# Kernel tuning notes

Hardware: AMD Instinct MI355X
Metric: run time of the kernel (lower is better)

## Reference

```python
import jax, jax.numpy as jnp
import numpy as np

N_NODES = 50000
N_EDGES = 1200000
F_IN = 128
F_EDGE = 32
H = 78


def _p(key, shape, fan_in):
    return jax.random.normal(key, shape, dtype=jnp.float32) / np.sqrt(fan_in)


def setup_inputs() -> dict:
    key = jax.random.key(0)
    ks = jax.random.split(key, 20)
    x = jax.random.normal(ks[0], (N_NODES, F_IN), dtype=jnp.float32)
    edge_index = jax.random.randint(ks[1], (2, N_EDGES), 0, N_NODES, dtype=jnp.int32)
    edge_attr = jax.random.normal(ks[2], (N_EDGES, F_EDGE), dtype=jnp.float32)
    return {
        "x": x, "edge_index": edge_index, "edge_attr": edge_attr,
        # GATConv layer 1
        "W1": _p(ks[3], (F_IN, H), F_IN), "as1": _p(ks[4], (H,), H), "ad1": _p(ks[5], (H,), H),
        "b1": jnp.zeros((H,), jnp.float32),
        # GATConv layer 2
        "W2": _p(ks[6], (H, H), H), "as2": _p(ks[7], (H,), H), "ad2": _p(ks[8], (H,), H),
        "b2": jnp.zeros((H,), jnp.float32),
        # edge MLP
        "Wm1": _p(ks[9], (F_EDGE, H), F_EDGE), "bm1": jnp.zeros((H,), jnp.float32),
        "Wm2": _p(ks[10], (H, H), H), "bm2": jnp.zeros((H,), jnp.float32),
        # final edge head
        "Wf": _p(ks[11], (3 * H, 1), 3 * H), "bf": jnp.zeros((1,), jnp.float32),
    }


def _gat_conv(x, W, a_src, a_dst, bias, src, dst, n_nodes):
    """PyG GATConv, heads=1, negative_slope=0.2, self-loops already in src/dst."""
    h = x @ W                                   # [N, H]
    alpha_s = h @ a_src                         # [N]
    alpha_d = h @ a_dst                         # [N]
    e = jax.nn.leaky_relu(alpha_s[src] + alpha_d[dst], negative_slope=0.2)  # [E']
    # softmax over incoming edges per destination node
    m = jax.ops.segment_max(e, dst, num_segments=n_nodes)
    e = jnp.exp(e - m[dst])
    s = jax.ops.segment_sum(e, dst, num_segments=n_nodes)
    alpha = e / (s[dst] + 1e-16)                # [E']
    out = jax.ops.segment_sum(alpha[:, None] * h[src], dst, num_segments=n_nodes)
    return out + bias


def reference(x, edge_index, edge_attr, W1, as1, ad1, b1, W2, as2, ad2, b2,
              Wm1, bm1, Wm2, bm2, Wf, bf):
    n_nodes = x.shape[0]
    loop = jnp.arange(n_nodes, dtype=edge_index.dtype)
    src = jnp.concatenate([edge_index[0], loop])  # add self-loops (PyG default)
    dst = jnp.concatenate([edge_index[1], loop])

    h = _gat_conv(x, W1, as1, ad1, b1, src, dst, n_nodes)
    h = jax.nn.relu(h)  # dropout is identity in eval mode
    h = _gat_conv(h, W2, as2, ad2, b2, src, dst, n_nodes)

    ef = jax.nn.relu(edge_attr @ Wm1 + bm1) @ Wm2 + bm2            # [E, H]
    emb = jnp.concatenate([h[edge_index[0]], h[edge_index[1]], ef], axis=1)  # [E, 3H]
    return jnp.squeeze(emb @ Wf + bf, axis=-1)                     # [E]
```

## Files before the change

kernel.cpp:

```cpp
#include <hip/hip_runtime.h>
#include <math.h>

#define NN 50000
#define NE 1200000
#define FIN 128
#define FE 32
#define H 78
#define HP 80
#define ETOT (NE + NN)

#define NPB 64
#define NBUCK ((NN + NPB - 1) / NPB)
#define BCAP 2560

#define EB 6400
#define NBE ((ETOT + EB - 1) / EB)
#define GHN (NBUCK * NBE)
#define GS_NB ((GHN + 1023) / 1024)

typedef __attribute__((ext_vector_type(8))) short bf16x8;
typedef __attribute__((ext_vector_type(4))) float f32x4;

__device__ __forceinline__ unsigned short f2bf(float f) {
  unsigned u = __float_as_uint(f);
  return (unsigned short)((u + 0x7FFFu + ((u >> 16) & 1u)) >> 16);
}
__device__ __forceinline__ float bf2f(unsigned short b) {
  return __uint_as_float((unsigned)b << 16);
}

union Frag { uint4 q; bf16x8 v; unsigned short u[8]; };

__global__ void wperm_build(const float* __restrict__ W, int K, int steps,
                            uint4* __restrict__ out) {
  int idx = blockIdx.x * blockDim.x + threadIdx.x;
  int total = steps * 5 * 2 * 64;
  if (idx >= total) return;
  int lane = idx & 63;
  int fid = idx >> 6;
  int split = fid & 1;
  int sg = fid >> 1;
  int step = sg / 5, g = sg % 5;
  int kg = lane >> 4, l15 = lane & 15;
  int col = g * 16 + l15;
  Frag f;
#pragma unroll
  for (int e = 0; e < 8; ++e) {
    int k = step * 32 + kg * 8 + e;
    float v = (k < K && col < H) ? W[(size_t)k * H + col] : 0.f;
    unsigned short h = f2bf(v);
    if (split) h = f2bf(v - bf2f(h));
    f.u[e] = h;
  }
  out[idx] = f.q;
}

template<int STEPS, int LDA>
__global__ __launch_bounds__(256)
void gemm_mfma(const float* __restrict__ A, const uint4* __restrict__ wperm,
               const float* __restrict__ as, const float* __restrict__ ad,
               unsigned* __restrict__ hb, float* __restrict__ asv,
               float* __restrict__ adv) {
  int lane = threadIdx.x & 63;
  int gw = blockIdx.x * 4 + (threadIdx.x >> 6);
  int n0w = gw * 16;
  if (n0w >= NN) return;
  int l15 = lane & 15, kg = lane >> 4;
  f32x4 acc[5];
#pragma unroll
  for (int g = 0; g < 5; ++g) acc[g] = (f32x4){0.f, 0.f, 0.f, 0.f};

#pragma unroll
  for (int step = 0; step < STEPS; ++step) {
    int k0 = step * 32 + kg * 8;
    bf16x8 ah, al;
    if (k0 < LDA) {
      int row = n0w + l15;
      if (row >= NN) row = NN - 1;
      const float* ar = A + (size_t)row * LDA + k0;
      float4 f0 = *reinterpret_cast<const float4*>(ar);
      float4 f1 = *reinterpret_cast<const float4*>(ar + 4);
      float fv[8] = {f0.x, f0.y, f0.z, f0.w, f1.x, f1.y, f1.z, f1.w};
#pragma unroll
      for (int e = 0; e < 8; ++e) {
        unsigned short h = f2bf(fv[e]);
        ah[e] = (short)h;
        al[e] = (short)f2bf(fv[e] - bf2f(h));
      }
    } else {
#pragma unroll
      for (int e = 0; e < 8; ++e) { ah[e] = 0; al[e] = 0; }
    }
#pragma unroll
    for (int g = 0; g < 5; ++g) {
      Frag wh, wl;
      wh.q = wperm[((size_t)(step * 5 + g) * 2 + 0) * 64 + lane];
      wl.q = wperm[((size_t)(step * 5 + g) * 2 + 1) * 64 + lane];
      acc[g] = __builtin_amdgcn_mfma_f32_16x16x32_bf16(ah, wh.v, acc[g], 0, 0, 0);
      acc[g] = __builtin_amdgcn_mfma_f32_16x16x32_bf16(al, wh.v, acc[g], 0, 0, 0);
      acc[g] = __builtin_amdgcn_mfma_f32_16x16x32_bf16(ah, wl.v, acc[g], 0, 0, 0);
    }
  }

  float asl[5], adl[5];
#pragma unroll
  for (int g = 0; g < 5; ++g) {
    int col = g * 16 + l15;
    asl[g] = (col < H) ? as[col] : 0.f;
    adl[g] = (col < H) ? ad[col] : 0.f;
  }

#pragma unroll
  for (int r = 0; r < 4; ++r) {
    int node = n0w + kg * 4 + r;
#pragma unroll
    for (int g = 0; g < 5; ++g) {
      float c = acc[g][r];
      float cn = __shfl_xor(c, 1);
      if (!(l15 & 1) && node < NN)
        hb[(size_t)node * (HP / 2) + g * 8 + (l15 >> 1)] =
            (unsigned)f2bf(c) | ((unsigned)f2bf(cn) << 16);
    }
    float sa = 0.f, sd = 0.f;
#pragma unroll
    for (int g = 0; g < 5; ++g) {
      sa = fmaf(acc[g][r], asl[g], sa);
      sd = fmaf(acc[g][r], adl[g], sd);
    }
#pragma unroll
    for (int mask = 1; mask < 16; mask <<= 1) {
      sa += __shfl_xor(sa, mask);
      sd += __shfl_xor(sd, mask);
    }
    if (l15 == 0 && node < NN) { asv[node] = sa; adv[node] = sd; }
  }
}

__global__ __launch_bounds__(256)
void bin_hist(const int* __restrict__ ei, int* __restrict__ gh) {
  __shared__ int hist[NBUCK];
  int b = blockIdx.x, t = threadIdx.x;
  for (int k = t; k < NBUCK; k += 256) hist[k] = 0;
  __syncthreads();
  int e0 = b * EB;
  int e1 = min(e0 + EB, ETOT);
  for (int i = e0 + t; i < e1; i += 256) {
    int dst = (i < NE) ? ei[NE + i] : (i - NE);
    atomicAdd(&hist[dst >> 6], 1);
  }
  __syncthreads();
  for (int k = t; k < NBUCK; k += 256) gh[(size_t)k * NBE + b] = hist[k];
}

__global__ void scan1g(const int* __restrict__ gh, int* __restrict__ gsum) {
  __shared__ int sh[256];
  int b = blockIdx.x, t = threadIdx.x;
  int i0 = b * 1024 + t * 4;
  int s = 0;
#pragma unroll
  for (int k = 0; k < 4; ++k) {
    int i = i0 + k;
    if (i < GHN) s += gh[i];
  }
  sh[t] = s;
  __syncthreads();
  for (int off = 128; off > 0; off >>= 1) {
    if (t < off) sh[t] += sh[t + off];
    __syncthreads();
  }
  if (t == 0) gsum[b] = sh[0];
}

__global__ void scan2g(const int* __restrict__ gsum, int* __restrict__ gboff) {
  __shared__ int sh[256];
  int t = threadIdx.x;
  sh[t] = (t < GS_NB) ? gsum[t] : 0;
  __syncthreads();
  for (int off = 1; off < 256; off <<= 1) {
    int v = (t >= off) ? sh[t - off] : 0;
    __syncthreads();
    sh[t] += v;
    __syncthreads();
  }
  if (t < GS_NB) gboff[t] = (t == 0) ? 0 : sh[t - 1];
}

__global__ void scan3g(const int* __restrict__ gh, const int* __restrict__ gboff,
                       int* __restrict__ goff) {
  __shared__ int sh[256];
  int b = blockIdx.x, t = threadIdx.x;
  int i0 = b * 1024 + t * 4;
  int v[4];
  int s = 0;
#pragma unroll
  for (int k = 0; k < 4; ++k) {
    int i = i0 + k;
    v[k] = (i < GHN) ? gh[i] : 0;
    s += v[k];
  }
  sh[t] = s;
  __syncthreads();
  for (int off = 1; off < 256; off <<= 1) {
    int u = (t >= off) ? sh[t - off] : 0;
    __syncthreads();
    sh[t] += u;
    __syncthreads();
  }
  int run = gboff[b] + ((t == 0) ? 0 : sh[t - 1]);
#pragma unroll
  for (int k = 0; k < 4; ++k) {
    int i = i0 + k;
    if (i < GHN) { goff[i] = run; run += v[k]; }
  }
}

__global__ __launch_bounds__(256)
void bin_place(const int* __restrict__ ei, const int* __restrict__ goff,
               unsigned long long* __restrict__ tmp) {
  __shared__ int cursor[NBUCK];
  int b = blockIdx.x, t = threadIdx.x;
  for (int k = t; k < NBUCK; k += 256) cursor[k] = goff[(size_t)k * NBE + b];
  __syncthreads();
  int e0 = b * EB;
  int e1 = min(e0 + EB, ETOT);
  for (int i = e0 + t; i < e1; i += 256) {
    int src, dst;
    if (i < NE) { src = ei[i]; dst = ei[NE + i]; }
    else { src = dst = i - NE; }
    int pos = atomicAdd(&cursor[dst >> 6], 1);
    tmp[pos] = ((unsigned long long)(unsigned)dst << 32) | (unsigned)src;
  }
}

__global__ __launch_bounds__(256)
void bucket_build(const unsigned long long* __restrict__ tmp,
                  const int* __restrict__ goff,
                  int* __restrict__ rowptr, int* __restrict__ srcs) {
  __shared__ int hist[NPB];
  __shared__ int offs[NPB];
  __shared__ int curs[NPB];
  __shared__ int srcs_l[BCAP];
  int b = blockIdx.x, t = threadIdx.x;
  int base = goff[(size_t)b * NBE];
  int next = (b + 1 < NBUCK) ? goff[(size_t)(b + 1) * NBE] : ETOT;
  int cnt = next - base;
  int n0 = b * NPB;
  if (t < NPB) hist[t] = 0;
  __syncthreads();
  for (int p = t; p < cnt; p += 256) {
    int dst = (int)(tmp[base + p] >> 32);
    atomicAdd(&hist[dst - n0], 1);
  }
  __syncthreads();
  if (t == 0) {
    int run = 0;
    for (int j = 0; j < NPB; ++j) { offs[j] = run; run += hist[j]; }
  }
  __syncthreads();
  if (t < NPB) {
    curs[t] = offs[t];
    int n = n0 + t;
    if (n < NN) rowptr[n] = base + offs[t];
  }
  if (b == NBUCK - 1 && t == 0) rowptr[NN] = ETOT;
  __syncthreads();
  for (int p = t; p < cnt; p += 256) {
    unsigned long long e = tmp[base + p];
    int dst = (int)(e >> 32);
    int src = (int)(e & 0xffffffffULL);
    int lp = atomicAdd(&curs[dst - n0], 1);
    if (lp < BCAP) srcs_l[lp] = src;
    else srcs[base + lp] = src;
  }
  __syncthreads();
  int m = cnt < BCAP ? cnt : BCAP;
  for (int p = t; p < m; p += 256) srcs[base + p] = srcs_l[p];
}

template<int RELU>
__global__ __launch_bounds__(256)
void gat_fused(const int* __restrict__ rowptr, const int* __restrict__ srcs,
               const float* __restrict__ asv, const float* __restrict__ adv,
               const unsigned* __restrict__ hb, const float* __restrict__ bias,
               float* __restrict__ outp) {
  int n = (blockIdx.x * 256 + threadIdx.x) >> 6;
  int lane = threadIdx.x & 63;
  if (n >= NN) return;
  int r0 = rowptr[n], r1 = rowptr[n + 1];
  int deg = r1 - r0;
  float advn = adv[n];

  int s0 = 0;
  float e0 = -INFINITY;
  if (lane < deg) {
    s0 = srcs[r0 + lane];
    float e = asv[s0] + advn;
    e0 = e > 0.f ? e : 0.2f * e;
  }
  float m = e0;
#pragma unroll
  for (int off = 1; off < 64; off <<= 1) m = fmaxf(m, __shfl_xor(m, off));
  float ssum = (lane < deg) ? __expf(e0 - m) : 0.f;
#pragma unroll
  for (int off = 1; off < 64; off <<= 1) ssum += __shfl_xor(ssum, off);
  for (int c = r0 + 64; c < r1; c += 64) {
    int p = c + lane;
    float e = -INFINITY;
    if (p < r1) {
      float t = asv[srcs[p]] + advn;
      e = t > 0.f ? t : 0.2f * t;
    }
    float cm = e;
#pragma unroll
    for (int off = 1; off < 64; off <<= 1) cm = fmaxf(cm, __shfl_xor(cm, off));
    float c2 = (p < r1) ? __expf(e - cm) : 0.f;
#pragma unroll
    for (int off = 1; off < 64; off <<= 1) c2 += __shfl_xor(c2, off);
    float mn = fmaxf(m, cm);
    ssum = ssum * __expf(m - mn) + c2 * __expf(cm - mn);
    m = mn;
  }
  float inv = 1.f / (ssum + 1e-16f);
  float alpha0 = (lane < deg) ? __expf(e0 - m) * inv : 0.f;

  int g3 = lane / 20;
  int lp = lane - g3 * 20;
  float4 acc = {0.f, 0.f, 0.f, 0.f};
  int nch = deg < 64 ? deg : 64;
  for (int base = 0; base < nch; base += 3) {
    int p = base + g3;
    bool act = (g3 < 3) && (p < nch);
    int idx = p < 63 ? p : 63;
    float al = __shfl(alpha0, idx);
    int s = __shfl(s0, idx);
    if (act) {
      const unsigned* hr = hb + (size_t)s * (HP / 2) + lp * 2;
      unsigned w0 = hr[0], w1 = hr[1];
      acc.x = fmaf(al, bf2f((unsigned short)(w0 & 0xffff)), acc.x);
      acc.y = fmaf(al, bf2f((unsigned short)(w0 >> 16)), acc.y);
      acc.z = fmaf(al, bf2f((unsigned short)(w1 & 0xffff)), acc.z);
      acc.w = fmaf(al, bf2f((unsigned short)(w1 >> 16)), acc.w);
    }
  }
  for (int c = r0 + 64; c < r1; c += 64) {
    int p = c + lane;
    float al = 0.f;
    int s = 0;
    if (p < r1) {
      s = srcs[p];
      float t = asv[s] + advn;
      t = t > 0.f ? t : 0.2f * t;
      al = __expf(t - m) * inv;
    }
    int cnt = min(r1 - c, 64);
    for (int base = 0; base < cnt; base += 3) {
      int p2 = base + g3;
      bool act = (g3 < 3) && (p2 < cnt);
      int idx = p2 < 63 ? p2 : 63;
      float alq = __shfl(al, idx);
      int sq = __shfl(s, idx);
      if (act) {
        const unsigned* hr = hb + (size_t)sq * (HP / 2) + lp * 2;
        unsigned w0 = hr[0], w1 = hr[1];
        acc.x = fmaf(alq, bf2f((unsigned short)(w0 & 0xffff)), acc.x);
        acc.y = fmaf(alq, bf2f((unsigned short)(w0 >> 16)), acc.y);
        acc.z = fmaf(alq, bf2f((unsigned short)(w1 & 0xffff)), acc.z);
        acc.w = fmaf(alq, bf2f((unsigned short)(w1 >> 16)), acc.w);
      }
    }
  }

  float4 a1, a2;
  a1.x = __shfl(acc.x, lane + 20); a1.y = __shfl(acc.y, lane + 20);
  a1.z = __shfl(acc.z, lane + 20); a1.w = __shfl(acc.w, lane + 20);
  a2.x = __shfl(acc.x, lane + 40); a2.y = __shfl(acc.y, lane + 40);
  a2.z = __shfl(acc.z, lane + 40); a2.w = __shfl(acc.w, lane + 40);
  if (lane < 20) {
    int c0 = lane * 4;
    float4 o;
    o.x = acc.x + a1.x + a2.x + ((c0 + 0 < H) ? bias[c0 + 0] : 0.f);
    o.y = acc.y + a1.y + a2.y + ((c0 + 1 < H) ? bias[c0 + 1] : 0.f);
    o.z = acc.z + a1.z + a2.z + ((c0 + 2 < H) ? bias[c0 + 2] : 0.f);
    o.w = acc.w + a1.w + a2.w + ((c0 + 3 < H) ? bias[c0 + 3] : 0.f);
    if (RELU) {
      o.x = fmaxf(o.x, 0.f); o.y = fmaxf(o.y, 0.f);
      o.z = fmaxf(o.z, 0.f); o.w = fmaxf(o.w, 0.f);
    }
    *reinterpret_cast<float4*>(outp + (size_t)n * HP + c0) = o;
  }
}

__global__ void final_node(const float* __restrict__ h2f, const float* __restrict__ Wf,
                           float* __restrict__ u, float* __restrict__ v) {
  int n = blockIdx.x * blockDim.x + threadIdx.x;
  if (n >= NN) return;
  const float* r = h2f + (size_t)n * HP;
  float su = 0.f, sv = 0.f;
#pragma unroll
  for (int j = 0; j < H; ++j) {
    float hv = r[j];
    su += hv * Wf[j];
    sv += hv * Wf[H + j];
  }
  u[n] = su;
  v[n] = sv;
}

__global__ void mk_wproj(const float* __restrict__ Wm2, const float* __restrict__ bm2,
                         const float* __restrict__ Wf, const float* __restrict__ bf,
                         float* __restrict__ wpc) {
  int k = threadIdx.x;
  if (k < H) {
    float s = 0.f;
    for (int j = 0; j < H; ++j) s += Wm2[k * H + j] * Wf[2 * H + j];
    wpc[k] = s;
  } else if (k == H) {
    float s = 0.f;
    for (int j = 0; j < H; ++j) s += bm2[j] * Wf[2 * H + j];
    wpc[H] = s + bf[0];
  }
}

#define FE_WAVES 18750
__global__ __launch_bounds__(256)
void final_edge_mfma(const int* __restrict__ ei, const float* __restrict__ ea,
                     const float* __restrict__ Wm1, const float* __restrict__ bm1,
                     const float* __restrict__ wpc, const float* __restrict__ u,
                     const float* __restrict__ v, float* __restrict__ out) {
  int lane = threadIdx.x & 63;
  long gw = (long)blockIdx.x * 4 + (threadIdx.x >> 6);
  if (gw >= FE_WAVES) return;
  int l15 = lane & 15;
  int kg = lane >> 4;
  bf16x8 bfrag[5];
  float bm1c[5], wpcc[5];
#pragma unroll
  for (int g = 0; g < 5; ++g) {
    int col = g * 16 + l15;
    bool valid = col < H;
    bm1c[g] = valid ? bm1[col] : 0.f;
    wpcc[g] = valid ? wpc[col] : 0.f;
#pragma unroll
    for (int e = 0; e < 8; ++e) {
      int kk = kg * 8 + e;
      bfrag[g][e] = valid ? (short)f2bf(Wm1[kk * H + col]) : (short)0;
    }
  }
  float basec = wpc[H];
  int e0 = (int)(gw * 64);
#pragma unroll
  for (int t = 0; t < 4; ++t) {
    int ebase = e0 + t * 16;
    const float* ar = ea + (size_t)(ebase + l15) * FE + kg * 8;
    float4 f0 = *reinterpret_cast<const float4*>(ar);
    float4 f1 = *reinterpret_cast<const float4*>(ar + 4);
    bf16x8 afrag;
    afrag[0] = (short)f2bf(f0.x); afrag[1] = (short)f2bf(f0.y);
    afrag[2] = (short)f2bf(f0.z); afrag[3] = (short)f2bf(f0.w);
    afrag[4] = (short)f2bf(f1.x); afrag[5] = (short)f2bf(f1.y);
    afrag[6] = (short)f2bf(f1.z); afrag[7] = (short)f2bf(f1.w);
    float es0 = 0.f, es1 = 0.f, es2 = 0.f, es3 = 0.f;
#pragma unroll
    for (int g = 0; g < 5; ++g) {
      f32x4 c = {0.f, 0.f, 0.f, 0.f};
      c = __builtin_amdgcn_mfma_f32_16x16x32_bf16(afrag, bfrag[g], c, 0, 0, 0);
      es0 = fmaf(fmaxf(c[0] + bm1c[g], 0.f), wpcc[g], es0);
      es1 = fmaf(fmaxf(c[1] + bm1c[g], 0.f), wpcc[g], es1);
      es2 = fmaf(fmaxf(c[2] + bm1c[g], 0.f), wpcc[g], es2);
      es3 = fmaf(fmaxf(c[3] + bm1c[g], 0.f), wpcc[g], es3);
    }
#pragma unroll
    for (int m = 1; m < 16; m <<= 1) {
      es0 += __shfl_xor(es0, m);
      es1 += __shfl_xor(es1, m);
      es2 += __shfl_xor(es2, m);
      es3 += __shfl_xor(es3, m);
    }
    if (l15 < 4) {
      float es = (l15 == 0) ? es0 : (l15 == 1) ? es1 : (l15 == 2) ? es2 : es3;
      int e = ebase + kg * 4 + l15;
      int s = ei[e], d = ei[NE + e];
      out[e] = es + u[s] + v[d] + basec;
    }
  }
}

extern "C" void kernel_launch(void* const* d_in, const int* in_sizes, int n_in,
                              void* d_out, int out_size, void* d_ws, size_t ws_size,
                              hipStream_t stream) {
  const float* x   = (const float*)d_in[0];
  const int*   ei  = (const int*)d_in[1];
  const float* ea  = (const float*)d_in[2];
  const float* W1  = (const float*)d_in[3];
  const float* as1 = (const float*)d_in[4];
  const float* ad1 = (const float*)d_in[5];
  const float* b1  = (const float*)d_in[6];
  const float* W2  = (const float*)d_in[7];
  const float* as2 = (const float*)d_in[8];
  const float* ad2 = (const float*)d_in[9];
  const float* b2  = (const float*)d_in[10];
  const float* Wm1 = (const float*)d_in[11];
  const float* bm1 = (const float*)d_in[12];
  const float* Wm2 = (const float*)d_in[13];
  const float* bm2 = (const float*)d_in[14];
  const float* Wf  = (const float*)d_in[15];
  const float* bf  = (const float*)d_in[16];
  float* out = (float*)d_out;

  float* w = (float*)d_ws;
  float* h1   = w; w += (size_t)NN * HP;
  float* bufB = w; w += (size_t)NN * HP;
  unsigned* hb = (unsigned*)w; w += (size_t)NN * (HP / 2);
  uint4* wperm1 = (uint4*)w; w += 4 * 40 * 64;
  uint4* wperm2 = (uint4*)w; w += 4 * 30 * 64;
  float* asv  = w; w += NN;
  float* adv  = w; w += NN;
  float* uu   = w; w += NN;
  float* vv   = w; w += NN;
  float* wpc  = w; w += HP;
  unsigned long long* tmp = (unsigned long long*)w; w += 2 * (size_t)ETOT;
  int* rowptr = (int*)w; w += NN + 1;
  int* srcs   = (int*)w; w += ETOT;
  int* gh     = (int*)w; w += GHN;
  int* goff   = (int*)w; w += GHN;
  int* gsum   = (int*)w; w += GS_NB;
  int* gboff  = (int*)w; w += GS_NB;

  const int B = 256;
  dim3 gN((NN + B - 1) / B);
  dim3 gG((NN + 63) / 64);
  dim3 gW((NN * 64 + B - 1) / B);
  dim3 gFE((FE_WAVES + 3) / 4);

  wperm_build<<<(40 * 64 + B - 1) / B, B, 0, stream>>>(W1, FIN, 4, wperm1);
  wperm_build<<<(30 * 64 + B - 1) / B, B, 0, stream>>>(W2, H, 3, wperm2);

  bin_hist<<<NBE, B, 0, stream>>>(ei, gh);
  scan1g<<<GS_NB, B, 0, stream>>>(gh, gsum);
  scan2g<<<1, B, 0, stream>>>(gsum, gboff);
  scan3g<<<GS_NB, B, 0, stream>>>(gh, gboff, goff);
  bin_place<<<NBE, B, 0, stream>>>(ei, goff, tmp);
  bucket_build<<<NBUCK, B, 0, stream>>>(tmp, goff, rowptr, srcs);

  gemm_mfma<4, FIN><<<gG, B, 0, stream>>>(x, wperm1, as1, ad1, hb, asv, adv);
  gat_fused<1><<<gW, B, 0, stream>>>(rowptr, srcs, asv, adv, hb, b1, bufB);

  gemm_mfma<3, HP><<<gG, B, 0, stream>>>(bufB, wperm2, as2, ad2, hb, asv, adv);
  gat_fused<0><<<gW, B, 0, stream>>>(rowptr, srcs, asv, adv, hb, b2, h1);
  final_node<<<gN, B, 0, stream>>>(h1, Wf, uu, vv);

  mk_wproj<<<1, 128, 0, stream>>>(Wm2, bm2, Wf, bf, wpc);
  final_edge_mfma<<<gFE, B, 0, stream>>>(ei, ea, Wm1, bm1, wpc, uu, vv, out);
}
```

Baseline: 231.3 us.

## Fuse final node projection into second GAT and merge weight prep kernels

The second GAT aggregation now computes the per-node u/v projections directly with a wave reduction. This removes the h1 buffer write, the separate final_node read and one launch. Weight permutation and the projected-weight kernels are merged into a single launch. The edge binning block size is halved, with the single-block scan enlarged to 512 threads to cover the larger histogram. Neighbor row loads use a single 64-bit load.

```diff
diff --git a/kernel.cpp b/kernel.cpp
--- a/kernel.cpp
+++ b/kernel.cpp
@@ -13,7 +13,7 @@
 #define NBUCK ((NN + NPB - 1) / NPB)
 #define BCAP 2560
 
-#define EB 6400
+#define EB 3200
 #define NBE ((ETOT + EB - 1) / EB)
 #define GHN (NBUCK * NBE)
 #define GS_NB ((GHN + 1023) / 1024)
@@ -31,11 +31,8 @@
 
 union Frag { uint4 q; bf16x8 v; unsigned short u[8]; };
 
-__global__ void wperm_build(const float* __restrict__ W, int K, int steps,
-                            uint4* __restrict__ out) {
-  int idx = blockIdx.x * blockDim.x + threadIdx.x;
-  int total = steps * 5 * 2 * 64;
-  if (idx >= total) return;
+__device__ __forceinline__ void wperm_one(const float* __restrict__ W, int K, int idx,
+                                          uint4* __restrict__ out) {
   int lane = idx & 63;
   int fid = idx >> 6;
   int split = fid & 1;
@@ -53,6 +50,31 @@
     f.u[e] = h;
   }
   out[idx] = f.q;
+}
+
+__global__ void prep_all(const float* __restrict__ W1, const float* __restrict__ W2,
+                         const float* __restrict__ Wm2, const float* __restrict__ bm2,
+                         const float* __restrict__ Wf, const float* __restrict__ bf,
+                         uint4* __restrict__ wperm1, uint4* __restrict__ wperm2,
+                         float* __restrict__ wpc) {
+  int b = blockIdx.x, t = threadIdx.x;
+  if (b < 10) {
+    wperm_one(W1, FIN, b * 256 + t, wperm1);
+  } else if (b < 18) {
+    int idx = (b - 10) * 256 + t;
+    if (idx < 30 * 64) wperm_one(W2, H, idx, wperm2);
+  } else {
+    int k = t;
+    if (k < H) {
+      float s = 0.f;
+      for (int j = 0; j < H; ++j) s += Wm2[k * H + j] * Wf[2 * H + j];
+      wpc[k] = s;
+    } else if (k == H) {
+      float s = 0.f;
+      for (int j = 0; j < H; ++j) s += bm2[j] * Wf[2 * H + j];
+      wpc[H] = s + bf[0];
+    }
+  }
 }
 
 template<int STEPS, int LDA>
@@ -172,11 +194,11 @@
 }
 
 __global__ void scan2g(const int* __restrict__ gsum, int* __restrict__ gboff) {
-  __shared__ int sh[256];
+  __shared__ int sh[512];
   int t = threadIdx.x;
   sh[t] = (t < GS_NB) ? gsum[t] : 0;
   __syncthreads();
-  for (int off = 1; off < 256; off <<= 1) {
+  for (int off = 1; off < 512; off <<= 1) {
     int v = (t >= off) ? sh[t - off] : 0;
     __syncthreads();
     sh[t] += v;
@@ -277,12 +299,13 @@
   for (int p = t; p < m; p += 256) srcs[base + p] = srcs_l[p];
 }
 
-template<int RELU>
+template<int RELU, int FINAL>
 __global__ __launch_bounds__(256)
 void gat_fused(const int* __restrict__ rowptr, const int* __restrict__ srcs,
                const float* __restrict__ asv, const float* __restrict__ adv,
                const unsigned* __restrict__ hb, const float* __restrict__ bias,
-               float* __restrict__ outp) {
+               const float* __restrict__ Wf, float* __restrict__ outp,
+               float* __restrict__ uu, float* __restrict__ vv) {
   int n = (blockIdx.x * 256 + threadIdx.x) >> 6;
   int lane = threadIdx.x & 63;
   if (n >= NN) return;
@@ -334,12 +357,11 @@
     float al = __shfl(alpha0, idx);
     int s = __shfl(s0, idx);
     if (act) {
-      const unsigned* hr = hb + (size_t)s * (HP / 2) + lp * 2;
-      unsigned w0 = hr[0], w1 = hr[1];
-      acc.x = fmaf(al, bf2f((unsigned short)(w0 & 0xffff)), acc.x);
-      acc.y = fmaf(al, bf2f((unsigned short)(w0 >> 16)), acc.y);
-      acc.z = fmaf(al, bf2f((unsigned short)(w1 & 0xffff)), acc.z);
-      acc.w = fmaf(al, bf2f((unsigned short)(w1 >> 16)), acc.w);
+      uint2 w01 = *reinterpret_cast<const uint2*>(hb + (size_t)s * (HP / 2) + lp * 2);
+      acc.x = fmaf(al, bf2f((unsigned short)(w01.x & 0xffff)), acc.x);
+      acc.y = fmaf(al, bf2f((unsigned short)(w01.x >> 16)), acc.y);
+      acc.z = fmaf(al, bf2f((unsigned short)(w01.y & 0xffff)), acc.z);
+      acc.w = fmaf(al, bf2f((unsigned short)(w01.y >> 16)), acc.w);
     }
   }
   for (int c = r0 + 64; c < r1; c += 64) {
@@ -360,12 +382,11 @@
       float alq = __shfl(al, idx);
       int sq = __shfl(s, idx);
       if (act) {
-        const unsigned* hr = hb + (size_t)sq * (HP / 2) + lp * 2;
-        unsigned w0 = hr[0], w1 = hr[1];
-        acc.x = fmaf(alq, bf2f((unsigned short)(w0 & 0xffff)), acc.x);
-        acc.y = fmaf(alq, bf2f((unsigned short)(w0 >> 16)), acc.y);
-        acc.z = fmaf(alq, bf2f((unsigned short)(w1 & 0xffff)), acc.z);
-        acc.w = fmaf(alq, bf2f((unsigned short)(w1 >> 16)), acc.w);
+        uint2 w01 = *reinterpret_cast<const uint2*>(hb + (size_t)sq * (HP / 2) + lp * 2);
+        acc.x = fmaf(alq, bf2f((unsigned short)(w01.x & 0xffff)), acc.x);
+        acc.y = fmaf(alq, bf2f((unsigned short)(w01.x >> 16)), acc.y);
+        acc.z = fmaf(alq, bf2f((unsigned short)(w01.y & 0xffff)), acc.z);
+        acc.w = fmaf(alq, bf2f((unsigned short)(w01.y >> 16)), acc.w);
       }
     }
   }
@@ -375,49 +396,46 @@
   a1.z = __shfl(acc.z, lane + 20); a1.w = __shfl(acc.w, lane + 20);
   a2.x = __shfl(acc.x, lane + 40); a2.y = __shfl(acc.y, lane + 40);
   a2.z = __shfl(acc.z, lane + 40); a2.w = __shfl(acc.w, lane + 40);
-  if (lane < 20) {
-    int c0 = lane * 4;
-    float4 o;
-    o.x = acc.x + a1.x + a2.x + ((c0 + 0 < H) ? bias[c0 + 0] : 0.f);
-    o.y = acc.y + a1.y + a2.y + ((c0 + 1 < H) ? bias[c0 + 1] : 0.f);
-    o.z = acc.z + a1.z + a2.z + ((c0 + 2 < H) ? bias[c0 + 2] : 0.f);
-    o.w = acc.w + a1.w + a2.w + ((c0 + 3 < H) ? bias[c0 + 3] : 0.f);
-    if (RELU) {
-      o.x = fmaxf(o.x, 0.f); o.y = fmaxf(o.y, 0.f);
-      o.z = fmaxf(o.z, 0.f); o.w = fmaxf(o.w, 0.f);
-    }
-    *reinterpret_cast<float4*>(outp + (size_t)n * HP + c0) = o;
-  }
-}
-
-__global__ void final_node(const float* __restrict__ h2f, const float* __restrict__ Wf,
-                           float* __restrict__ u, float* __restrict__ v) {
-  int n = blockIdx.x * blockDim.x + threadIdx.x;
-  if (n >= NN) return;
-  const float* r = h2f + (size_t)n * HP;
-  float su = 0.f, sv = 0.f;
-#pragma unroll
-  for (int j = 0; j < H; ++j) {
-    float hv = r[j];
-    su += hv * Wf[j];
-    sv += hv * Wf[H + j];
-  }
-  u[n] = su;
-  v[n] = sv;
-}
-
-__global__ void mk_wproj(const float* __restrict__ Wm2, const float* __restrict__ bm2,
-                         const float* __restrict__ Wf, const float* __restrict__ bf,
-                         float* __restrict__ wpc) {
-  int k = threadIdx.x;
-  if (k < H) {
-    float s = 0.f;
-    for (int j = 0; j < H; ++j) s += Wm2[k * H + j] * Wf[2 * H + j];
-    wpc[k] = s;
-  } else if (k == H) {
-    float s = 0.f;
-    for (int j = 0; j < H; ++j) s += bm2[j] * Wf[2 * H + j];
-    wpc[H] = s + bf[0];
+
+  if (FINAL) {
+    float su = 0.f, sv = 0.f;
+    if (lane < 20) {
+      int c0 = lane * 4;
+      float o0 = acc.x + a1.x + a2.x + ((c0 + 0 < H) ? bias[c0 + 0] : 0.f);
+      float o1 = acc.y + a1.y + a2.y + ((c0 + 1 < H) ? bias[c0 + 1] : 0.f);
+      float o2 = acc.z + a1.z + a2.z + ((c0 + 2 < H) ? bias[c0 + 2] : 0.f);
+      float o3 = acc.w + a1.w + a2.w + ((c0 + 3 < H) ? bias[c0 + 3] : 0.f);
+      float wu0 = (c0 + 0 < H) ? Wf[c0 + 0] : 0.f;
+      float wu1 = (c0 + 1 < H) ? Wf[c0 + 1] : 0.f;
+      float wu2 = (c0 + 2 < H) ? Wf[c0 + 2] : 0.f;
+      float wu3 = (c0 + 3 < H) ? Wf[c0 + 3] : 0.f;
+      float wv0 = (c0 + 0 < H) ? Wf[H + c0 + 0] : 0.f;
+      float wv1 = (c0 + 1 < H) ? Wf[H + c0 + 1] : 0.f;
+      float wv2 = (c0 + 2 < H) ? Wf[H + c0 + 2] : 0.f;
+      float wv3 = (c0 + 3 < H) ? Wf[H + c0 + 3] : 0.f;
+      su = o0 * wu0 + o1 * wu1 + o2 * wu2 + o3 * wu3;
+      sv = o0 * wv0 + o1 * wv1 + o2 * wv2 + o3 * wv3;
+    }
+#pragma unroll
+    for (int off = 1; off < 64; off <<= 1) {
+      su += __shfl_xor(su, off);
+      sv += __shfl_xor(sv, off);
+    }
+    if (lane == 0) { uu[n] = su; vv[n] = sv; }
+  } else {
+    if (lane < 20) {
+      int c0 = lane * 4;
+      float4 o;
+      o.x = acc.x + a1.x + a2.x + ((c0 + 0 < H) ? bias[c0 + 0] : 0.f);
+      o.y = acc.y + a1.y + a2.y + ((c0 + 1 < H) ? bias[c0 + 1] : 0.f);
+      o.z = acc.z + a1.z + a2.z + ((c0 + 2 < H) ? bias[c0 + 2] : 0.f);
+      o.w = acc.w + a1.w + a2.w + ((c0 + 3 < H) ? bias[c0 + 3] : 0.f);
+      if (RELU) {
+        o.x = fmaxf(o.x, 0.f); o.y = fmaxf(o.y, 0.f);
+        o.z = fmaxf(o.z, 0.f); o.w = fmaxf(o.w, 0.f);
+      }
+      *reinterpret_cast<float4*>(outp + (size_t)n * HP + c0) = o;
+    }
   }
 }
 
@@ -508,7 +526,6 @@
   float* out = (float*)d_out;
 
   float* w = (float*)d_ws;
-  float* h1   = w; w += (size_t)NN * HP;
   float* bufB = w; w += (size_t)NN * HP;
   unsigned* hb = (unsigned*)w; w += (size_t)NN * (HP / 2);
   uint4* wperm1 = (uint4*)w; w += 4 * 40 * 64;
@@ -527,28 +544,26 @@
   int* gboff  = (int*)w; w += GS_NB;
 
   const int B = 256;
-  dim3 gN((NN + B - 1) / B);
   dim3 gG((NN + 63) / 64);
   dim3 gW((NN * 64 + B - 1) / B);
   dim3 gFE((FE_WAVES + 3) / 4);
 
-  wperm_build<<<(40 * 64 + B - 1) / B, B, 0, stream>>>(W1, FIN, 4, wperm1);
-  wperm_build<<<(30 * 64 + B - 1) / B, B, 0, stream>>>(W2, H, 3, wperm2);
+  prep_all<<<19, B, 0, stream>>>(W1, W2, Wm2, bm2, Wf, bf, wperm1, wperm2, wpc);
 
   bin_hist<<<NBE, B, 0, stream>>>(ei, gh);
   scan1g<<<GS_NB, B, 0, stream>>>(gh, gsum);
-  scan2g<<<1, B, 0, stream>>>(gsum, gboff);
+  scan2g<<<1, 512, 0, stream>>>(gsum, gboff);
   scan3g<<<GS_NB, B, 0, stream>>>(gh, gboff, goff);
   bin_place<<<NBE, B, 0, stream>>>(ei, goff, tmp);
   bucket_build<<<NBUCK, B, 0, stream>>>(tmp, goff, rowptr, srcs);
 
   gemm_mfma<4, FIN><<<gG, B, 0, stream>>>(x, wperm1, as1, ad1, hb, asv, adv);
-  gat_fused<1><<<gW, B, 0, stream>>>(rowptr, srcs, asv, adv, hb, b1, bufB);
+  gat_fused<1, 0><<<gW, B, 0, stream>>>(rowptr, srcs, asv, adv, hb, b1, Wf,
+                                        bufB, uu, vv);
 
   gemm_mfma<3, HP><<<gG, B, 0, stream>>>(bufB, wperm2, as2, ad2, hb, asv, adv);
-  gat_fused<0><<<gW, B, 0, stream>>>(rowptr, srcs, asv, adv, hb, b2, h1);
-  final_node<<<gN, B, 0, stream>>>(h1, Wf, uu, vv);
-
-  mk_wproj<<<1, 128, 0, stream>>>(Wm2, bm2, Wf, bf, wpc);
+  gat_fused<0, 1><<<gW, B, 0, stream>>>(rowptr, srcs, asv, adv, hb, b2, Wf,
+                                        nullptr, uu, vv);
+
   final_edge_mfma<<<gFE, B, 0, stream>>>(ei, ea, Wm1, bm1, wpc, uu, vv, out);
 }
```

New measurement: 216.8 us. 1.07x faster.
